# Kernel optimization log

Hardware: AMD Instinct MI355X
Metric: run time of the kernel (lower is better)

## Reference

```python
import jax, jax.numpy as jnp
import numpy as np

NUM_HEADS = 16
ROPE_THETA = 10000.0


def _rope_cos_sin(seq_len, head_dim, dtype):
    # Llama rotary embedding: inv_freq over even dims, emb = cat(freqs, freqs)
    inv_freq = 1.0 / (ROPE_THETA ** (jnp.arange(0, head_dim, 2, dtype=jnp.float32) / head_dim))
    t = jnp.arange(seq_len, dtype=jnp.float32)
    freqs = jnp.outer(t, inv_freq)              # [S, hd/2]
    emb = jnp.concatenate([freqs, freqs], -1)   # [S, hd]
    return jnp.cos(emb).astype(dtype), jnp.sin(emb).astype(dtype)


def _rotate_half(x):
    h = x.shape[-1] // 2
    return jnp.concatenate([-x[..., h:], x[..., :h]], axis=-1)


def setup_inputs() -> dict:
    key = jax.random.key(0)
    ks = jax.random.split(key, 5)
    B, S, D = 1, 2048, 2048
    scale = 0.02
    return {
        "hidden_states": jax.random.normal(ks[0], (B, S, D), jnp.float32),
        "Wq": jax.random.normal(ks[1], (D, D), jnp.float32) * scale,
        "Wk": jax.random.normal(ks[2], (D, D), jnp.float32) * scale,
        "Wv": jax.random.normal(ks[3], (D, D), jnp.float32) * scale,
        "Wo": jax.random.normal(ks[4], (D, D), jnp.float32) * scale,
    }


def reference(hidden_states, Wq, Wk, Wv, Wo):
    B, S, D = hidden_states.shape
    H = NUM_HEADS
    hd = D // H
    sm_scale = 1.0 / np.sqrt(hd)

    # QKV projections (nn.Linear without bias: x @ W.T), kept in [B,S,H,hd]
    q = (hidden_states @ Wq.T).reshape(B, S, H, hd)
    k = (hidden_states @ Wk.T).reshape(B, S, H, hd)
    v = (hidden_states @ Wv.T).reshape(B, S, H, hd)

    # RoPE (offset=0, no kv cache)
    cos, sin = _rope_cos_sin(S, hd, hidden_states.dtype)
    cos = cos[None, :, None, :]  # [1,S,1,hd]
    sin = sin[None, :, None, :]
    q = q * cos + _rotate_half(q) * sin
    k = k * cos + _rotate_half(k) * sin

    # Causal self-attention (exact math of FlashSelfAttention(causal=True))
    scores = jnp.einsum("bshd,bthd->bhst", q, k) * sm_scale  # [B,H,S,S]
    causal = jnp.tril(jnp.ones((S, S), dtype=bool))
    scores = jnp.where(causal[None, None], scores, jnp.finfo(scores.dtype).min)
    probs = jax.nn.softmax(scores, axis=-1)
    attn = jnp.einsum("bhst,bthd->bshd", probs, v)           # [B,S,H,hd]

    # Output projection
    attn = attn.reshape(B, S, H * hd)
    return attn @ Wo.T
```

## Files before the change

### kernel.cpp

```cpp
#include <hip/hip_runtime.h>
#include <hip/hip_bf16.h>
#include <math.h>

#define S_LEN 2048
#define DMODEL 2048
#define NHEADS 16
#define HDIM 128

typedef __bf16 bf16x8 __attribute__((ext_vector_type(8)));
typedef float f32x4 __attribute__((ext_vector_type(4)));
typedef float f32x16 __attribute__((ext_vector_type(16)));

__device__ __forceinline__ unsigned short f2b(float f) {
  union { float f; unsigned u; } c; c.f = f;
  unsigned r = (c.u + 0x7fffu + ((c.u >> 16) & 1u)) >> 16;
  return (unsigned short)r;
}
__device__ __forceinline__ float b2f(unsigned short b) {
  union { unsigned u; float f; } c; c.u = ((unsigned)b) << 16;
  return c.f;
}

__device__ __forceinline__ void gload_lds16(const unsigned short* g, unsigned short* l) {
  __builtin_amdgcn_global_load_lds(
      (__attribute__((address_space(1))) void*)(void*)g,
      (__attribute__((address_space(3))) void*)(void*)l, 16, 0, 0);
}

__global__ void cvt5_f32_bf16_k(const float* __restrict__ s0,
                                const float* __restrict__ s1,
                                const float* __restrict__ s2,
                                const float* __restrict__ s3,
                                const float* __restrict__ s4,
                                unsigned short* __restrict__ d0,
                                unsigned short* __restrict__ d1,
                                unsigned short* __restrict__ d2,
                                unsigned short* __restrict__ d3,
                                unsigned short* __restrict__ d4) {
  int gi = blockIdx.x * blockDim.x + threadIdx.x;
  int seg = gi >> 20;
  int i = (gi & 0xFFFFF) * 4;
  const float* src = (seg == 0) ? s0 : (seg == 1) ? s1 : (seg == 2) ? s2
                     : (seg == 3) ? s3 : s4;
  unsigned short* dst = (seg == 0) ? d0 : (seg == 1) ? d1 : (seg == 2) ? d2
                        : (seg == 3) ? d3 : d4;
  float4 v = *reinterpret_cast<const float4*>(src + i);
  ushort4 o;
  o.x = f2b(v.x); o.y = f2b(v.y); o.z = f2b(v.z); o.w = f2b(v.w);
  *reinterpret_cast<ushort4*>(dst + i) = o;
}

__global__ void addf2_k(const float* __restrict__ a, const float* __restrict__ b,
                        float* __restrict__ out) {
  int i = (blockIdx.x * blockDim.x + threadIdx.x) * 4;
  float4 x = *reinterpret_cast<const float4*>(a + i);
  float4 y = *reinterpret_cast<const float4*>(b + i);
  x.x += y.x; x.y += y.y; x.z += y.z; x.w += y.w;
  *reinterpret_cast<float4*>(out + i) = x;
}

__global__ void rope_table_k(float* __restrict__ cs, float* __restrict__ sn) {
  int idx = blockIdx.x * blockDim.x + threadIdx.x;
  int s = idx >> 6, i = idx & 63;
  float inv = powf(10000.0f, -(float)(2 * i) / 128.0f);
  float a = (float)s * inv;
  cs[idx] = cosf(a);
  sn[idx] = sinf(a);
}

__global__ void rope_apply_k(unsigned short* __restrict__ q,
                             unsigned short* __restrict__ k,
                             const float* __restrict__ cs,
                             const float* __restrict__ sn) {
  const float SC = 0.08838834764831845f * 1.4426950408889634f;
  int idx = blockIdx.x * blockDim.x + threadIdx.x;
  int i = idx & 63;
  int h = (idx >> 6) & (NHEADS - 1);
  int s = idx >> 10;
  size_t base = (size_t)s * DMODEL + h * HDIM;
  float c = cs[s * 64 + i], sv = sn[s * 64 + i];
  float qc = c * SC, qs = sv * SC;
  float q1 = b2f(q[base + i]), q2 = b2f(q[base + i + 64]);
  q[base + i]      = f2b(q1 * qc - q2 * qs);
  q[base + i + 64] = f2b(q2 * qc + q1 * qs);
  float k1 = b2f(k[base + i]), k2 = b2f(k[base + i + 64]);
  k[base + i]      = f2b(k1 * c - k2 * sv);
  k[base + i + 64] = f2b(k2 * c + k1 * sv);
}

__global__ __launch_bounds__(256) void transpose_bf16_k(
    const unsigned short* __restrict__ in, unsigned short* __restrict__ out) {
  __shared__ unsigned short tile[64][72];
  int bx = blockIdx.x, by = blockIdx.y;
  int t = threadIdx.x;
#pragma unroll
  for (int i = 0; i < 2; ++i) {
    int ch = i * 256 + t;
    int r = ch >> 3, c8 = ch & 7;
    bf16x8 v = *reinterpret_cast<const bf16x8*>(
        in + (size_t)(by * 64 + r) * DMODEL + bx * 64 + c8 * 8);
    *reinterpret_cast<bf16x8*>(&tile[r][c8 * 8]) = v;
  }
  __syncthreads();
#pragma unroll
  for (int i = 0; i < 2; ++i) {
    int ch = i * 256 + t;
    int c = ch >> 3, r8 = ch & 7;
    union { bf16x8 v; unsigned short u[8]; } w;
#pragma unroll
    for (int j = 0; j < 8; ++j) w.u[j] = tile[r8 * 8 + j][c];
    *reinterpret_cast<bf16x8*>(
        out + (size_t)(bx * 64 + c) * S_LEN + by * 64 + r8 * 8) = w.v;
  }
}


#define MIDBAR_SEQ()                                      \
  do {                                                    \
    asm volatile("" ::: "memory");                        \
    __builtin_amdgcn_s_barrier();                         \
    asm volatile("s_waitcnt lgkmcnt(0)" ::: "memory");    \
    __builtin_amdgcn_sched_barrier(0);                    \
    __builtin_amdgcn_s_setprio(1);                        \
  } while (0)

#define ENDBAR_SEQ()                                      \
  do {                                                    \
    __builtin_amdgcn_s_setprio(0);                        \
    asm volatile("" ::: "memory");                        \
    __builtin_amdgcn_s_barrier();                         \
    asm volatile("" ::: "memory");                        \
  } while (0)

#define READA(QM)                                                              \
  do {                                                                         \
    _Pragma("unroll") for (int j = 0; j < MQ; ++j)                             \
    _Pragma("unroll") for (int kk = 0; kk < 2; ++kk) {                         \
      int row = wm * (BM / 2) + ((QM) * MQ + j) * 16 + li;                     \
      int c = (kk * 4 + g) ^ (li & 7);                                         \
      af[j][kk] = *reinterpret_cast<const bf16x8*>(&As[cur][row * 64 + c * 8]);\
    }                                                                          \
  } while (0)

#define READB(BF, QN)                                                          \
  do {                                                                         \
    _Pragma("unroll") for (int jn = 0; jn < 2; ++jn)                           \
    _Pragma("unroll") for (int kk = 0; kk < 2; ++kk) {                         \
      int row = wn * 64 + ((QN) * 2 + jn) * 16 + li;                           \
      int c = (kk * 4 + g) ^ (li & 7);                                         \
      BF[jn][kk] = *reinterpret_cast<const bf16x8*>(&Bs[cur][row * 64 + c * 8]);\
    }                                                                          \
  } while (0)

#define QUAD(QM, QN, BF)                                                       \
  do {                                                                         \
    _Pragma("unroll") for (int j = 0; j < MQ; ++j)                             \
    _Pragma("unroll") for (int jn = 0; jn < 2; ++jn)                           \
    _Pragma("unroll") for (int kk = 0; kk < 2; ++kk)                           \
      acc[(QM) * MQ + j][(QN) * 2 + jn] =                                      \
          __builtin_amdgcn_mfma_f32_16x16x32_bf16(                             \
              af[j][kk], BF[jn][kk], acc[(QM) * MQ + j][(QN) * 2 + jn], 0, 0, 0);\
  } while (0)

template <int BM, bool OUT_F32>
__global__ __launch_bounds__(512, 2) void gemm_8ph_k(
    const unsigned short* __restrict__ A, const unsigned short* __restrict__ B0p,
    const unsigned short* __restrict__ B1p, const unsigned short* __restrict__ B2p,
    void* __restrict__ C0, void* __restrict__ C1, void* __restrict__ C2,
    int M, int N, int Kl, int Kstr, int aoffz) {
  constexpr int MQ = BM / 64;
  constexpr int MR = BM / 32;

  __shared__ unsigned short As[2][BM * 64];
  __shared__ unsigned short Bs[2][256 * 64];

  const unsigned short* Ap = A + (size_t)blockIdx.z * aoffz;
  const unsigned short* Bp = (blockIdx.z == 0) ? B0p : (blockIdx.z == 1) ? B1p : B2p;
  void* Cout = (blockIdx.z == 0) ? C0 : (blockIdx.z == 1) ? C1 : C2;

  int nwg = gridDim.x, bid = blockIdx.x;
  int wg = (bid & 7) * (nwg >> 3) + (bid >> 3);
  int ntn = N >> 8;
  int tm = wg / ntn, tn = wg % ntn;
  int m0 = tm * BM, n0 = tn << 8;

  const int tid = threadIdx.x;
  const int wave = tid >> 6, lane = tid & 63;
  const int g = lane >> 4, li = lane & 15;
  const int wm = wave >> 2, wn = wave & 3;

  auto stageB = [&](int buf, int tt, int qn) {
#pragma unroll
    for (int i = 0; i < 2; ++i) {
      int j = i * 512 + tid;
      int piece = j >> 8, rowin = (j >> 3) & 31, c = j & 7;
      int row = piece * 64 + qn * 32 + rowin;
      gload_lds16(Bp + (size_t)(n0 + row) * Kstr + tt * 64 + ((c ^ (row & 7)) * 8),
                  &Bs[buf][row * 64 + c * 8]);
    }
  };
  auto stageA = [&](int buf, int tt, int qm) {
#pragma unroll
    for (int i = 0; i < BM / 128; ++i) {
      int j = i * 512 + tid;
      int piece = j / (2 * BM);
      int rowin = (j >> 3) & (BM / 4 - 1);
      int c = j & 7;
      int row = piece * (BM / 2) + qm * (BM / 4) + rowin;
      gload_lds16(Ap + (size_t)(m0 + row) * Kstr + tt * 64 + ((c ^ (row & 7)) * 8),
                  &As[buf][row * 64 + c * 8]);
    }
  };

  f32x4 acc[MR][4];
#pragma unroll
  for (int i = 0; i < MR; ++i)
#pragma unroll
    for (int j = 0; j < 4; ++j) acc[i][j] = (f32x4){0.f, 0.f, 0.f, 0.f};

  const int nK = Kl >> 6;

  stageB(0, 0, 0); stageA(0, 0, 0); stageB(0, 0, 1); stageA(0, 0, 1);
  stageB(1, 1, 0); stageA(1, 1, 0); stageB(1, 1, 1); stageA(1, 1, 1);
  if constexpr (BM == 256) asm volatile("s_waitcnt vmcnt(8)" ::: "memory");
  else                     asm volatile("s_waitcnt vmcnt(6)" ::: "memory");
  asm volatile("" ::: "memory");
  __builtin_amdgcn_s_barrier();
  asm volatile("" ::: "memory");

  for (int t = 0; t < nK; ++t) {
    int cur = t & 1;
    bool pf = (t + 2 < nK);
    bf16x8 af[MQ][2], bf0[2][2], bf1[2][2];
    READA(0);
    READB(bf0, 0);
    MIDBAR_SEQ();
    QUAD(0, 0, bf0);
    ENDBAR_SEQ();
    READB(bf1, 1);
    if (pf) { stageB(cur, t + 2, 0); stageA(cur, t + 2, 0); }
    MIDBAR_SEQ();
    QUAD(0, 1, bf1);
    ENDBAR_SEQ();
    READA(1);
    if (pf) stageB(cur, t + 2, 1);
    MIDBAR_SEQ();
    QUAD(1, 1, bf1);
    ENDBAR_SEQ();
    if (pf) {
      stageA(cur, t + 2, 1);
      if constexpr (BM == 256) asm volatile("s_waitcnt vmcnt(8)" ::: "memory");
      else                     asm volatile("s_waitcnt vmcnt(6)" ::: "memory");
    } else {
      asm volatile("s_waitcnt vmcnt(0)" ::: "memory");
    }
    MIDBAR_SEQ();
    QUAD(1, 0, bf0);
    ENDBAR_SEQ();
  }

#pragma unroll
  for (int m = 0; m < MR; ++m) {
#pragma unroll
    for (int n = 0; n < 4; ++n) {
      int row = m0 + wm * (BM / 2) + m * 16 + g * 4;
      int col = n0 + wn * 64 + n * 16 + li;
#pragma unroll
      for (int r = 0; r < 4; ++r) {
        if (OUT_F32)
          reinterpret_cast<float*>(Cout)[(size_t)(row + r) * N + col] = acc[m][n][r];
        else
          reinterpret_cast<unsigned short*>(Cout)[(size_t)(row + r) * N + col] =
              f2b(acc[m][n][r]);
      }
    }
  }
}

#undef MIDBAR_SEQ
#undef ENDBAR_SEQ
#undef READA
#undef READB
#undef QUAD

__global__ __launch_bounds__(256) void flash_attn_k(
    const unsigned short* __restrict__ q, const unsigned short* __restrict__ k,
    const unsigned short* __restrict__ vt, unsigned short* __restrict__ o) {
  __shared__ unsigned short Ks[2][2][64 * 128];
  __shared__ unsigned short Vs[2][2][128 * 64];

  int L = blockIdx.x;
  int xcd = L & 7, j = L >> 3;
  int h = 2 * xcd + (j & 1);
  int qt = (j < 32) ? (31 - (j >> 1)) : ((j - 32) >> 1);

  int t = threadIdx.x, wave = t >> 6, l = t & 63;
  int l5 = l >> 5, l31 = l & 31;
  int par = wave >> 1, qh = wave & 1;
  int q0 = qt * 64;
  int q_abs = q0 + qh * 32 + l31;

  const unsigned short* vth = vt + (size_t)h * HDIM * S_LEN;

  auto stage = [&](int buf, int itv) {
#pragma unroll
    for (int p2 = 0; p2 < 2; ++p2) {
      int kv0 = (2 * itv + p2) * 64;
#pragma unroll
      for (int i = 0; i < 4; ++i) {
        int ch = i * 256 + t;
        int row = ch >> 4, c = ch & 15;
        gload_lds16(k + (size_t)(kv0 + row) * DMODEL + h * HDIM + ((c ^ (row & 7)) * 8),
                    &Ks[p2][buf][ch * 8]);
      }
#pragma unroll
      for (int i = 0; i < 4; ++i) {
        int ch = i * 256 + t;
        int row = ch >> 3, c = ch & 7;
        gload_lds16(vth + (size_t)row * S_LEN + kv0 + ((c ^ (row & 7)) * 8),
                    &Vs[p2][buf][ch * 8]);
      }
    }
  };

  bf16x8 qf[8];
#pragma unroll
  for (int kb = 0; kb < 8; ++kb)
    qf[kb] = *reinterpret_cast<const bf16x8*>(
        q + (size_t)q_abs * DMODEL + h * HDIM + kb * 16 + l5 * 8);

  f32x16 OT[4];
#pragma unroll
  for (int nf = 0; nf < 4; ++nf)
#pragma unroll
    for (int r = 0; r < 16; ++r) OT[nf][r] = 0.f;
  float m_r = -1e30f, l_r = 0.f;

  int nIter = (qt >> 1) + 1;
  stage(0, 0);

  for (int it = 0; it < nIter; ++it) {
    int cur = it & 1;
    if (it + 1 < nIter) {
      stage(cur ^ 1, it + 1);
      asm volatile("s_waitcnt vmcnt(16)" ::: "memory");
    } else {
      asm volatile("s_waitcnt vmcnt(0)" ::: "memory");
    }
    __builtin_amdgcn_s_barrier();
    asm volatile("" ::: "memory");

    int myt = 2 * it + par;
    if (myt <= qt) {
      int kv0 = myt * 64;
      f32x16 sf[2];
#pragma unroll
      for (int kvs = 0; kvs < 2; ++kvs)
#pragma unroll
        for (int r = 0; r < 16; ++r) sf[kvs][r] = 0.f;
#pragma unroll
      for (int kb = 0; kb < 8; ++kb) {
#pragma unroll
        for (int kvs = 0; kvs < 2; ++kvs) {
          int row = kvs * 32 + l31;
          int c = (2 * kb + l5) ^ (row & 7);
          bf16x8 kf = *reinterpret_cast<const bf16x8*>(&Ks[par][cur][row * 128 + c * 8]);
          sf[kvs] = __builtin_amdgcn_mfma_f32_32x32x16_bf16(kf, qf[kb], sf[kvs], 0, 0, 0);
        }
      }
      if (myt == qt) {
#pragma unroll
        for (int kvs = 0; kvs < 2; ++kvs)
#pragma unroll
          for (int r = 0; r < 16; ++r) {
            int kv_abs = kv0 + kvs * 32 + (r & 3) + 8 * (r >> 2) + 4 * l5;
            if (kv_abs > q_abs) sf[kvs][r] = -1e30f;
          }
      }
      float pm = -1e30f;
#pragma unroll
      for (int kvs = 0; kvs < 2; ++kvs)
#pragma unroll
        for (int r = 0; r < 16; ++r) pm = fmaxf(pm, sf[kvs][r]);
      pm = fmaxf(pm, __shfl_xor(pm, 32));
      float nm = fmaxf(m_r, pm);
      float alpha = exp2f(m_r - nm);
      m_r = nm;
      float ls = 0.f;
#pragma unroll
      for (int kvs = 0; kvs < 2; ++kvs)
#pragma unroll
        for (int r = 0; r < 16; ++r) {
          float pv = exp2f(sf[kvs][r] - nm);
          sf[kvs][r] = pv;
          ls += pv;
        }
      l_r = l_r * alpha + ls + __shfl_xor(ls, 32);
#pragma unroll
      for (int nf = 0; nf < 4; ++nf)
#pragma unroll
        for (int r = 0; r < 16; ++r) OT[nf][r] *= alpha;

      bf16x8 pf[4];
#pragma unroll
      for (int ks = 0; ks < 4; ++ks) {
        const int kvs = ks >> 1;
        const int m0 = 8 * (ks & 1);
        unsigned A0, A1, B0, B1;
        asm("v_cvt_pk_bf16_f32 %0, %1, %2" : "=v"(A0) : "v"(sf[kvs][m0 + 0]), "v"(sf[kvs][m0 + 1]));
        asm("v_cvt_pk_bf16_f32 %0, %1, %2" : "=v"(A1) : "v"(sf[kvs][m0 + 2]), "v"(sf[kvs][m0 + 3]));
        asm("v_cvt_pk_bf16_f32 %0, %1, %2" : "=v"(B0) : "v"(sf[kvs][m0 + 4]), "v"(sf[kvs][m0 + 5]));
        asm("v_cvt_pk_bf16_f32 %0, %1, %2" : "=v"(B1) : "v"(sf[kvs][m0 + 6]), "v"(sf[kvs][m0 + 7]));
        unsigned rA0 = (unsigned)__shfl_xor((int)A0, 32);
        unsigned rA1 = (unsigned)__shfl_xor((int)A1, 32);
        unsigned rB0 = (unsigned)__shfl_xor((int)B0, 32);
        unsigned rB1 = (unsigned)__shfl_xor((int)B1, 32);
        union { unsigned u[4]; bf16x8 v; } pk;
        pk.u[0] = l5 ? rB0 : A0;
        pk.u[1] = l5 ? rB1 : A1;
        pk.u[2] = l5 ? B0 : rA0;
        pk.u[3] = l5 ? B1 : rA1;
        pf[ks] = pk.v;
      }

#pragma unroll
      for (int ks = 0; ks < 4; ++ks) {
#pragma unroll
        for (int nf = 0; nf < 4; ++nf) {
          int row = nf * 32 + l31;
          int c = (2 * ks + l5) ^ (row & 7);
          bf16x8 vf = *reinterpret_cast<const bf16x8*>(&Vs[par][cur][row * 64 + c * 8]);
          OT[nf] = __builtin_amdgcn_mfma_f32_32x32x16_bf16(vf, pf[ks], OT[nf], 0, 0, 0);
        }
      }
    }
    __builtin_amdgcn_s_barrier();
    asm volatile("" ::: "memory");
  }

  float* MS = (float*)&Ks[0][0][0];
  float* ML = MS + 8192;
  if (par == 1) {
#pragma unroll
    for (int nf = 0; nf < 4; ++nf)
#pragma unroll
      for (int r = 0; r < 16; ++r) {
        int d = nf * 32 + (r & 3) + 8 * (r >> 2) + 4 * l5;
        MS[qh * 4096 + d * 32 + l31] = OT[nf][r];
      }
    if (l < 32) { ML[qh * 64 + l31] = m_r; ML[qh * 64 + 32 + l31] = l_r; }
  }
  __builtin_amdgcn_s_barrier();
  asm volatile("" ::: "memory");
  if (par == 0) {
    float mB = ML[qh * 64 + l31], lB = ML[qh * 64 + 32 + l31];
    float ms = fmaxf(m_r, mB);
    float eA = exp2f(m_r - ms), eB = exp2f(mB - ms);
    float inv = 1.0f / (l_r * eA + lB * eB);
#pragma unroll
    for (int nf = 0; nf < 4; ++nf)
#pragma unroll
      for (int r = 0; r < 16; ++r) {
        int d = nf * 32 + (r & 3) + 8 * (r >> 2) + 4 * l5;
        OT[nf][r] = (OT[nf][r] * eA + MS[qh * 4096 + d * 32 + l31] * eB) * inv;
      }
  }
  __builtin_amdgcn_s_barrier();
  asm volatile("" ::: "memory");
  if (par == 0) {
#pragma unroll
    for (int nf = 0; nf < 4; ++nf)
#pragma unroll
      for (int r = 0; r < 16; ++r) {
        int d = nf * 32 + (r & 3) + 8 * (r >> 2) + 4 * l5;
        MS[qh * 4096 + d * 32 + l31] = OT[nf][r];
      }
  }
  __builtin_amdgcn_s_barrier();
  asm volatile("" ::: "memory");
  {
    int qq = t >> 2;
    int dg = (t & 3) * 32;
    const float* src = MS + (qq >> 5) * 4096 + (qq & 31);
    unsigned pk[16];
#pragma unroll
    for (int i = 0; i < 16; ++i) {
      unsigned lo = f2b(src[(dg + 2 * i) * 32]);
      unsigned hi = f2b(src[(dg + 2 * i + 1) * 32]);
      pk[i] = lo | (hi << 16);
    }
    unsigned short* op = o + (size_t)(q0 + qq) * DMODEL + h * HDIM + dg;
#pragma unroll
    for (int i = 0; i < 4; ++i) {
      uint4 w = make_uint4(pk[4 * i], pk[4 * i + 1], pk[4 * i + 2], pk[4 * i + 3]);
      *reinterpret_cast<uint4*>(op + i * 8) = w;
    }
  }
}

extern "C" void kernel_launch(void* const* d_in, const int* in_sizes, int n_in,
                              void* d_out, int out_size, void* d_ws, size_t ws_size,
                              hipStream_t stream) {
  const float* hs = (const float*)d_in[0];
  const float* Wq = (const float*)d_in[1];
  const float* Wk = (const float*)d_in[2];
  const float* Wv = (const float*)d_in[3];
  const float* Wo = (const float*)d_in[4];

  char* ws = (char*)d_ws;
  const size_t MB = 1024 * 1024;
  unsigned short* hs_b = (unsigned short*)(ws + 0 * MB);
  unsigned short* Wq_b = (unsigned short*)(ws + 8 * MB);
  unsigned short* Wk_b = (unsigned short*)(ws + 16 * MB);
  unsigned short* Wv_b = (unsigned short*)(ws + 24 * MB);
  unsigned short* Wo_b = (unsigned short*)(ws + 32 * MB);
  unsigned short* qb = (unsigned short*)(ws + 40 * MB);
  unsigned short* kb = (unsigned short*)(ws + 48 * MB);
  unsigned short* vb = (unsigned short*)(ws + 56 * MB);
  unsigned short* ab = (unsigned short*)(ws + 64 * MB);
  float* cs = (float*)(ws + 72 * MB);
  float* sn = (float*)(ws + 72 * MB + 512 * 1024);
  unsigned short* vtb = hs_b;
  float* P0 = (float*)(ws + 8 * MB);
  float* P1 = (float*)(ws + 40 * MB);

  cvt5_f32_bf16_k<<<(5 * 1024 * 1024) / 256, 256, 0, stream>>>(
      hs, Wq, Wk, Wv, Wo, hs_b, Wq_b, Wk_b, Wv_b, Wo_b);

  rope_table_k<<<(S_LEN * 64) / 256, 256, 0, stream>>>(cs, sn);

  gemm_8ph_k<256, false><<<dim3(64, 1, 3), 512, 0, stream>>>(
      hs_b, Wq_b, Wk_b, Wv_b, qb, kb, vb, 2048, 2048, 2048, 2048, 0);

  transpose_bf16_k<<<dim3(32, 32), 256, 0, stream>>>(vb, vtb);

  rope_apply_k<<<(S_LEN * NHEADS * 64) / 256, 256, 0, stream>>>(qb, kb, cs, sn);

  flash_attn_k<<<dim3(512), 256, 0, stream>>>(qb, kb, vtb, ab);

  gemm_8ph_k<128, true><<<dim3(128, 1, 2), 512, 0, stream>>>(
      ab, Wo_b, Wo_b + 1024, Wo_b, P0, P1, P0, 2048, 2048, 1024, 2048, 1024);
  addf2_k<<<(2048 * 2048) / 1024, 256, 0, stream>>>(P0, P1, (float*)d_out);
}
```

Before: 206.2 us.

## Split KV work per wave pair into 32-row halves of each 64-row tile

Each iteration now covers one 64-row KV tile split into two 32-row halves, one per wave pair, instead of two 64-row tiles alternated between pairs. This removes the idle pair on the last odd iteration and halves the LDS footprint, which may allow higher occupancy. In exchange the loop runs twice as many iterations, with more barriers and less MFMA work between syncs. The causal mask now applies per 32-row half on the diagonal tile.

```diff
diff --git a/kernel.cpp b/kernel.cpp
--- a/kernel.cpp
+++ b/kernel.cpp
@@ -286,8 +286,8 @@
 __global__ __launch_bounds__(256) void flash_attn_k(
     const unsigned short* __restrict__ q, const unsigned short* __restrict__ k,
     const unsigned short* __restrict__ vt, unsigned short* __restrict__ o) {
-  __shared__ unsigned short Ks[2][2][64 * 128];
-  __shared__ unsigned short Vs[2][2][128 * 64];
+  __shared__ unsigned short Ks[2][2][32 * 128];
+  __shared__ unsigned short Vs[2][2][128 * 32];
 
   int L = blockIdx.x;
   int xcd = L & 7, j = L >> 3;
@@ -302,22 +302,22 @@
 
   const unsigned short* vth = vt + (size_t)h * HDIM * S_LEN;
 
-  auto stage = [&](int buf, int itv) {
+  auto stage = [&](int buf, int it) {
 #pragma unroll
     for (int p2 = 0; p2 < 2; ++p2) {
-      int kv0 = (2 * itv + p2) * 64;
-#pragma unroll
-      for (int i = 0; i < 4; ++i) {
+      int kv0 = it * 64 + p2 * 32;
+#pragma unroll
+      for (int i = 0; i < 2; ++i) {
         int ch = i * 256 + t;
         int row = ch >> 4, c = ch & 15;
         gload_lds16(k + (size_t)(kv0 + row) * DMODEL + h * HDIM + ((c ^ (row & 7)) * 8),
                     &Ks[p2][buf][ch * 8]);
       }
 #pragma unroll
-      for (int i = 0; i < 4; ++i) {
+      for (int i = 0; i < 2; ++i) {
         int ch = i * 256 + t;
-        int row = ch >> 3, c = ch & 7;
-        gload_lds16(vth + (size_t)row * S_LEN + kv0 + ((c ^ (row & 7)) * 8),
+        int row = ch >> 2, c = ch & 3;
+        gload_lds16(vth + (size_t)row * S_LEN + kv0 + ((c ^ (row & 3)) * 8),
                     &Vs[p2][buf][ch * 8]);
       }
     }
@@ -336,102 +336,86 @@
     for (int r = 0; r < 16; ++r) OT[nf][r] = 0.f;
   float m_r = -1e30f, l_r = 0.f;
 
-  int nIter = (qt >> 1) + 1;
+  int nIter = qt + 1;
   stage(0, 0);
 
   for (int it = 0; it < nIter; ++it) {
     int cur = it & 1;
     if (it + 1 < nIter) {
       stage(cur ^ 1, it + 1);
-      asm volatile("s_waitcnt vmcnt(16)" ::: "memory");
+      asm volatile("s_waitcnt vmcnt(8)" ::: "memory");
     } else {
       asm volatile("s_waitcnt vmcnt(0)" ::: "memory");
     }
     __builtin_amdgcn_s_barrier();
     asm volatile("" ::: "memory");
 
-    int myt = 2 * it + par;
-    if (myt <= qt) {
-      int kv0 = myt * 64;
-      f32x16 sf[2];
-#pragma unroll
-      for (int kvs = 0; kvs < 2; ++kvs)
-#pragma unroll
-        for (int r = 0; r < 16; ++r) sf[kvs][r] = 0.f;
-#pragma unroll
-      for (int kb = 0; kb < 8; ++kb) {
-#pragma unroll
-        for (int kvs = 0; kvs < 2; ++kvs) {
-          int row = kvs * 32 + l31;
-          int c = (2 * kb + l5) ^ (row & 7);
-          bf16x8 kf = *reinterpret_cast<const bf16x8*>(&Ks[par][cur][row * 128 + c * 8]);
-          sf[kvs] = __builtin_amdgcn_mfma_f32_32x32x16_bf16(kf, qf[kb], sf[kvs], 0, 0, 0);
-        }
-      }
-      if (myt == qt) {
-#pragma unroll
-        for (int kvs = 0; kvs < 2; ++kvs)
-#pragma unroll
-          for (int r = 0; r < 16; ++r) {
-            int kv_abs = kv0 + kvs * 32 + (r & 3) + 8 * (r >> 2) + 4 * l5;
-            if (kv_abs > q_abs) sf[kvs][r] = -1e30f;
-          }
-      }
-      float pm = -1e30f;
-#pragma unroll
-      for (int kvs = 0; kvs < 2; ++kvs)
-#pragma unroll
-        for (int r = 0; r < 16; ++r) pm = fmaxf(pm, sf[kvs][r]);
-      pm = fmaxf(pm, __shfl_xor(pm, 32));
-      float nm = fmaxf(m_r, pm);
-      float alpha = exp2f(m_r - nm);
-      m_r = nm;
-      float ls = 0.f;
-#pragma unroll
-      for (int kvs = 0; kvs < 2; ++kvs)
-#pragma unroll
-        for (int r = 0; r < 16; ++r) {
-          float pv = exp2f(sf[kvs][r] - nm);
-          sf[kvs][r] = pv;
-          ls += pv;
-        }
-      l_r = l_r * alpha + ls + __shfl_xor(ls, 32);
-#pragma unroll
-      for (int nf = 0; nf < 4; ++nf)
-#pragma unroll
-        for (int r = 0; r < 16; ++r) OT[nf][r] *= alpha;
-
-      bf16x8 pf[4];
-#pragma unroll
-      for (int ks = 0; ks < 4; ++ks) {
-        const int kvs = ks >> 1;
-        const int m0 = 8 * (ks & 1);
-        unsigned A0, A1, B0, B1;
-        asm("v_cvt_pk_bf16_f32 %0, %1, %2" : "=v"(A0) : "v"(sf[kvs][m0 + 0]), "v"(sf[kvs][m0 + 1]));
-        asm("v_cvt_pk_bf16_f32 %0, %1, %2" : "=v"(A1) : "v"(sf[kvs][m0 + 2]), "v"(sf[kvs][m0 + 3]));
-        asm("v_cvt_pk_bf16_f32 %0, %1, %2" : "=v"(B0) : "v"(sf[kvs][m0 + 4]), "v"(sf[kvs][m0 + 5]));
-        asm("v_cvt_pk_bf16_f32 %0, %1, %2" : "=v"(B1) : "v"(sf[kvs][m0 + 6]), "v"(sf[kvs][m0 + 7]));
-        unsigned rA0 = (unsigned)__shfl_xor((int)A0, 32);
-        unsigned rA1 = (unsigned)__shfl_xor((int)A1, 32);
-        unsigned rB0 = (unsigned)__shfl_xor((int)B0, 32);
-        unsigned rB1 = (unsigned)__shfl_xor((int)B1, 32);
-        union { unsigned u[4]; bf16x8 v; } pk;
-        pk.u[0] = l5 ? rB0 : A0;
-        pk.u[1] = l5 ? rB1 : A1;
-        pk.u[2] = l5 ? B0 : rA0;
-        pk.u[3] = l5 ? B1 : rA1;
-        pf[ks] = pk.v;
-      }
-
-#pragma unroll
-      for (int ks = 0; ks < 4; ++ks) {
-#pragma unroll
-        for (int nf = 0; nf < 4; ++nf) {
-          int row = nf * 32 + l31;
-          int c = (2 * ks + l5) ^ (row & 7);
-          bf16x8 vf = *reinterpret_cast<const bf16x8*>(&Vs[par][cur][row * 64 + c * 8]);
-          OT[nf] = __builtin_amdgcn_mfma_f32_32x32x16_bf16(vf, pf[ks], OT[nf], 0, 0, 0);
-        }
+    int kv0 = it * 64 + par * 32;
+    f32x16 sf;
+#pragma unroll
+    for (int r = 0; r < 16; ++r) sf[r] = 0.f;
+#pragma unroll
+    for (int kb = 0; kb < 8; ++kb) {
+      int c = (2 * kb + l5) ^ (l31 & 7);
+      bf16x8 kf = *reinterpret_cast<const bf16x8*>(&Ks[par][cur][(l31 * 16 + c) * 8]);
+      sf = __builtin_amdgcn_mfma_f32_32x32x16_bf16(kf, qf[kb], sf, 0, 0, 0);
+    }
+    if (it == qt) {
+#pragma unroll
+      for (int r = 0; r < 16; ++r) {
+        int kv_abs = kv0 + (r & 3) + 8 * (r >> 2) + 4 * l5;
+        if (kv_abs > q_abs) sf[r] = -1e30f;
+      }
+    }
+    float pm = -1e30f;
+#pragma unroll
+    for (int r = 0; r < 16; ++r) pm = fmaxf(pm, sf[r]);
+    pm = fmaxf(pm, __shfl_xor(pm, 32));
+    float nm = fmaxf(m_r, pm);
+    float alpha = exp2f(m_r - nm);
+    m_r = nm;
+    float ls = 0.f;
+#pragma unroll
+    for (int r = 0; r < 16; ++r) {
+      float pv = exp2f(sf[r] - nm);
+      sf[r] = pv;
+      ls += pv;
+    }
+    l_r = l_r * alpha + ls + __shfl_xor(ls, 32);
+#pragma unroll
+    for (int nf = 0; nf < 4; ++nf)
+#pragma unroll
+      for (int r = 0; r < 16; ++r) OT[nf][r] *= alpha;
+
+    bf16x8 pf[2];
+#pragma unroll
+    for (int ks = 0; ks < 2; ++ks) {
+      const int m0 = 8 * ks;
+      unsigned A0, A1, B0, B1;
+      asm("v_cvt_pk_bf16_f32 %0, %1, %2" : "=v"(A0) : "v"(sf[m0 + 0]), "v"(sf[m0 + 1]));
+      asm("v_cvt_pk_bf16_f32 %0, %1, %2" : "=v"(A1) : "v"(sf[m0 + 2]), "v"(sf[m0 + 3]));
+      asm("v_cvt_pk_bf16_f32 %0, %1, %2" : "=v"(B0) : "v"(sf[m0 + 4]), "v"(sf[m0 + 5]));
+      asm("v_cvt_pk_bf16_f32 %0, %1, %2" : "=v"(B1) : "v"(sf[m0 + 6]), "v"(sf[m0 + 7]));
+      unsigned rA0 = (unsigned)__shfl_xor((int)A0, 32);
+      unsigned rA1 = (unsigned)__shfl_xor((int)A1, 32);
+      unsigned rB0 = (unsigned)__shfl_xor((int)B0, 32);
+      unsigned rB1 = (unsigned)__shfl_xor((int)B1, 32);
+      union { unsigned u[4]; bf16x8 v; } pk;
+      pk.u[0] = l5 ? rB0 : A0;
+      pk.u[1] = l5 ? rB1 : A1;
+      pk.u[2] = l5 ? B0 : rA0;
+      pk.u[3] = l5 ? B1 : rA1;
+      pf[ks] = pk.v;
+    }
+
+#pragma unroll
+    for (int ks = 0; ks < 2; ++ks) {
+#pragma unroll
+      for (int nf = 0; nf < 4; ++nf) {
+        int row = nf * 32 + l31;
+        int c = (2 * ks + l5) ^ (row & 3);
+        bf16x8 vf = *reinterpret_cast<const bf16x8*>(&Vs[par][cur][(row * 4 + c) * 8]);
+        OT[nf] = __builtin_amdgcn_mfma_f32_32x32x16_bf16(vf, pf[ks], OT[nf], 0, 0, 0);
       }
     }
     __builtin_amdgcn_s_barrier();
```

After: 204.3 us. Within noise of the previous version (-0.9%).
